# Kernel tuning notes

Hardware: AMD Instinct MI355X
Metric: run time of the kernel (lower is better)

## Reference

```python
import jax, jax.numpy as jnp
import numpy as np

N, D, R, NB = 50000, 128, 10, 4  # nodes, hidden, relations(with reverse), bases
E, NC = 800000, 12
LN_EPS = 1e-5


def _ln(x, g, b):
    m = x.mean(-1, keepdims=True)
    v = ((x - m) ** 2).mean(-1, keepdims=True)
    return (x - m) / jnp.sqrt(v + LN_EPS) * g + b


def _rgcn_conv(x, comp, bases, root, bias, src, dst, etype):
    # basis decomposition: W[r] = sum_b comp[r,b] * bases[b]
    W = jnp.einsum('rb,bio->rio', comp, bases)            # [R, D, D]
    xt = jnp.einsum('ni,rio->rno', x, W)                  # [R, N, D]
    msg = xt[etype, src]                                  # [E, D] gather
    seg = etype * N + dst                                 # per-(relation, dst) segments
    sums = jax.ops.segment_sum(msg, seg, num_segments=R * N)
    cnt = jax.ops.segment_sum(jnp.ones((msg.shape[0],), x.dtype), seg, num_segments=R * N)
    mean = sums / jnp.maximum(cnt, 1.0)[:, None]          # per-relation mean aggregation
    agg = mean.reshape(R, N, D).sum(0)                    # sum over relations
    return agg + x @ root + bias


def setup_inputs() -> dict:
    key = jax.random.key(0)
    ks = jax.random.split(key, 24)
    s = 0.02
    inp = {
        'edge_index': jax.random.randint(ks[0], (2, E), 0, N),
        'edge_type': jax.random.randint(ks[1], (E,), 0, R),
        'node_indices': jax.random.randint(ks[2], (8192,), 0, N),
        'file_feats': jax.random.normal(ks[3], (20000, 256), jnp.float32),
        'file_idx': jnp.arange(20000, dtype=jnp.int64),
        'domain_feats': jax.random.normal(ks[4], (15000, 128), jnp.float32),
        'domain_idx': jnp.arange(20000, 35000, dtype=jnp.int64),
        'ip_feats': jax.random.normal(ks[5], (10000, 64), jnp.float32),
        'ip_idx': jnp.arange(35000, 45000, dtype=jnp.int64),
        'fallback_emb': jax.random.normal(ks[6], (N, D), jnp.float32) * s,
        'Wf': jax.random.normal(ks[7], (256, D), jnp.float32) * s, 'bf': jnp.zeros((D,), jnp.float32),
        'Wd': jax.random.normal(ks[8], (128, D), jnp.float32) * s, 'bd': jnp.zeros((D,), jnp.float32),
        'Wi': jax.random.normal(ks[9], (64, D), jnp.float32) * s, 'bi': jnp.zeros((D,), jnp.float32),
        'comp1': jax.random.normal(ks[10], (R, NB), jnp.float32) * s,
        'bases1': jax.random.normal(ks[11], (NB, D, D), jnp.float32) * s,
        'root1': jax.random.normal(ks[12], (D, D), jnp.float32) * s, 'bias1': jnp.zeros((D,), jnp.float32),
        'comp2': jax.random.normal(ks[13], (R, NB), jnp.float32) * s,
        'bases2': jax.random.normal(ks[14], (NB, D, D), jnp.float32) * s,
        'root2': jax.random.normal(ks[15], (D, D), jnp.float32) * s, 'bias2': jnp.zeros((D,), jnp.float32),
        'ln1_g': jnp.ones((D,), jnp.float32), 'ln1_b': jnp.zeros((D,), jnp.float32),
        'ln2_g': jnp.ones((D,), jnp.float32), 'ln2_b': jnp.zeros((D,), jnp.float32),
        'Wc1': jax.random.normal(ks[16], (D, D), jnp.float32) * s, 'bc1': jnp.zeros((D,), jnp.float32),
        'Wc2': jax.random.normal(ks[17], (D, NC), jnp.float32) * s, 'bc2': jnp.zeros((NC,), jnp.float32),
    }
    return inp


def reference(edge_index, edge_type, node_indices, file_feats, file_idx, domain_feats,
              domain_idx, ip_feats, ip_idx, fallback_emb, Wf, bf, Wd, bd, Wi, bi,
              comp1, bases1, root1, bias1, comp2, bases2, root2, bias2,
              ln1_g, ln1_b, ln2_g, ln2_b, Wc1, bc1, Wc2, bc2):
    src, dst = edge_index[0], edge_index[1]
    # build node features: fallback embedding overwritten by typed projections
    x = fallback_emb
    x = x.at[file_idx].set(file_feats @ Wf + bf)
    x = x.at[domain_idx].set(domain_feats @ Wd + bd)
    x = x.at[ip_idx].set(ip_feats @ Wi + bi)
    h = _rgcn_conv(x, comp1, bases1, root1, bias1, src, dst, edge_type)
    h = jax.nn.relu(_ln(h, ln1_g, ln1_b))  # dropout is identity at eval
    h = _rgcn_conv(h, comp2, bases2, root2, bias2, src, dst, edge_type)
    h = _ln(h, ln2_g, ln2_b)
    h = h[node_indices]
    h = jax.nn.relu(h @ Wc1 + bc1)
    return h @ Wc2 + bc2
```

## Files before the change

kernel.cpp:

```cpp
#include <hip/hip_runtime.h>

#define D 128
#define R_REL 10
#define NBASE 4
#define NC 12
#define LN_EPS 1e-5f

typedef __attribute__((ext_vector_type(8))) short short8;
typedef __attribute__((ext_vector_type(4))) float f32x4;

static __device__ __forceinline__ unsigned short f2bf(float f) {
    unsigned u = __float_as_uint(f);
    unsigned r = (u + 0x7FFFu + ((u >> 16) & 1u)) >> 16;
    return (unsigned short)r;
}

__global__ void k_copy_bf(const float4* __restrict__ src, uint2* __restrict__ dst, int n4) {
    int i = blockIdx.x * blockDim.x + threadIdx.x;
    if (i < n4) {
        float4 v = src[i];
        uint2 o;
        o.x = (unsigned)f2bf(v.x) | ((unsigned)f2bf(v.y) << 16);
        o.y = (unsigned)f2bf(v.z) | ((unsigned)f2bf(v.w) << 16);
        dst[i] = o;
    }
}

__global__ void k_proj8(const float* __restrict__ feats, const float* __restrict__ W,
                        const float* __restrict__ bias, const int* __restrict__ idx,
                        unsigned short* __restrict__ xb, int M, int K) {
    __shared__ float lds[8 * 256];
    int m0 = blockIdx.x * 8;
    int rows = M - m0; if (rows > 8) rows = 8;
    for (int i = threadIdx.x; i < rows * K; i += 128) {
        int r = i / K, k = i - r * K;
        lds[r * K + k] = feats[(size_t)(m0 + r) * K + k];
    }
    __syncthreads();
    int o = threadIdx.x;
    float bz = bias[o];
    float acc[8];
#pragma unroll
    for (int r = 0; r < 8; ++r) acc[r] = bz;
    for (int k = 0; k < K; ++k) {
        float wv = W[k * D + o];
#pragma unroll
        for (int r = 0; r < 8; ++r) acc[r] = fmaf(lds[r * K + k], wv, acc[r]);
    }
#pragma unroll
    for (int r = 0; r < 8; ++r) {
        if (r < rows) xb[(size_t)idx[m0 + r] * D + o] = f2bf(acc[r]);
    }
}

__global__ void k_deg(const int* __restrict__ ei, int* __restrict__ deg, int E) {
    int e = blockIdx.x * blockDim.x + threadIdx.x;
    if (e < E) atomicAdd(&deg[ei[E + e]], 1);
}

#define SCAN_B 256
__global__ void k_scan1(const int* __restrict__ deg, int* __restrict__ off,
                        int* __restrict__ bsum, int n) {
    __shared__ int lds[SCAN_B];
    int i = blockIdx.x * SCAN_B + threadIdx.x;
    int v = (i < n) ? deg[i] : 0;
    lds[threadIdx.x] = v; __syncthreads();
    for (int s = 1; s < SCAN_B; s <<= 1) {
        int t = (threadIdx.x >= s) ? lds[threadIdx.x - s] : 0;
        __syncthreads();
        lds[threadIdx.x] += t;
        __syncthreads();
    }
    if (i < n) off[i] = lds[threadIdx.x] - v;
    if (threadIdx.x == SCAN_B - 1) bsum[blockIdx.x] = lds[threadIdx.x];
}
__global__ void k_scan2(int* __restrict__ bsum, int nb) {
    __shared__ int lds[SCAN_B];
    int v = (threadIdx.x < nb) ? bsum[threadIdx.x] : 0;
    lds[threadIdx.x] = v; __syncthreads();
    for (int s = 1; s < SCAN_B; s <<= 1) {
        int t = (threadIdx.x >= s) ? lds[threadIdx.x - s] : 0;
        __syncthreads();
        lds[threadIdx.x] += t;
        __syncthreads();
    }
    if (threadIdx.x < nb) bsum[threadIdx.x] = lds[threadIdx.x] - v;
}
__global__ void k_scan3(int* __restrict__ off, const int* __restrict__ bsum,
                        int* __restrict__ cursor, int n) {
    int i = blockIdx.x * SCAN_B + threadIdx.x;
    if (i < n) {
        int o = off[i] + bsum[blockIdx.x];
        off[i] = o;
        cursor[i] = o;
    }
}

__global__ void k_fill(const int* __restrict__ ei, const int* __restrict__ et,
                       int* __restrict__ cursor, unsigned* __restrict__ csr, int E) {
    int e = blockIdx.x * blockDim.x + threadIdx.x;
    if (e < E) {
        int d = ei[E + e];
        int p = atomicAdd(&cursor[d], 1);
        csr[p] = (unsigned)ei[e] | ((unsigned)et[e] << 16);
    }
}

__global__ void k_agg(const unsigned short* __restrict__ xb, const int* __restrict__ off,
                      const int* __restrict__ deg, const unsigned* __restrict__ csr,
                      const float* __restrict__ comp, unsigned short* __restrict__ Zb, int Nn) {
    __shared__ float acc[4][R_REL][D];
    __shared__ float scomp[R_REL * NBASE];
    int w = threadIdx.x >> 6;
    int lane = threadIdx.x & 63;
    if (threadIdx.x < R_REL * NBASE) scomp[threadIdx.x] = comp[threadIdx.x];
    for (int i = threadIdx.x; i < 4 * R_REL * D; i += 256) ((float*)acc)[i] = 0.f;
    __syncthreads();

    int n = blockIdx.x * 4 + w;
    if (n >= Nn) return;

    int start = off[n];
    int dg = deg[n];
    int myCnt = 0;
    float* accw = &acc[w][0][0];
    for (int j = 0; j < dg; ++j) {
        unsigned u = csr[start + j];
        int src = (int)(u & 0xFFFFu);
        int et = (int)(u >> 16);
        unsigned xv = *(const unsigned*)&xb[(size_t)src * D + lane * 2];
        float vx = __uint_as_float(xv << 16);
        float vy = __uint_as_float(xv & 0xFFFF0000u);
        float2 a = *(float2*)&accw[et * D + lane * 2];
        a.x += vx; a.y += vy;
        *(float2*)&accw[et * D + lane * 2] = a;
        if (lane == et) myCnt++;
    }
    float inv[R_REL];
#pragma unroll
    for (int r = 0; r < R_REL; ++r) {
        int c = __shfl(myCnt, r, 64);
        inv[r] = (c > 0) ? (1.f / (float)c) : 1.f;
    }
    float2 mean[R_REL];
#pragma unroll
    for (int r = 0; r < R_REL; ++r) {
        float2 a = *(float2*)&accw[r * D + lane * 2];
        mean[r].x = a.x * inv[r];
        mean[r].y = a.y * inv[r];
    }
#pragma unroll
    for (int b = 0; b < NBASE; ++b) {
        float zx = 0.f, zy = 0.f;
#pragma unroll
        for (int r = 0; r < R_REL; ++r) {
            float c = scomp[r * NBASE + b];
            zx = fmaf(c, mean[r].x, zx);
            zy = fmaf(c, mean[r].y, zy);
        }
        unsigned o = (unsigned)f2bf(zx) | ((unsigned)f2bf(zy) << 16);
        *(unsigned*)&Zb[(size_t)n * 512 + b * D + lane * 2] = o;
    }
}

__global__ void k_bt(const float* __restrict__ bases, const float* __restrict__ root,
                     unsigned short* __restrict__ BT) {
    int i = blockIdx.x * 256 + threadIdx.x;
    if (i >= 128 * 640) return;
    int n = i / 640, k = i - n * 640;
    float v = (k < 512) ? bases[(size_t)k * D + n] : root[(size_t)(k - 512) * D + n];
    BT[i] = f2bf(v);
}

__global__ void k_gemm_mfma(const unsigned short* __restrict__ Zb,
                            const unsigned short* __restrict__ xb,
                            const unsigned short* __restrict__ BT,
                            const float* __restrict__ bias,
                            float* __restrict__ P, int M) {
    __shared__ unsigned short As[32 * 40];
    __shared__ unsigned short Bs[128 * 40];
    int t = threadIdx.x;
    int l = t & 63;
    int w = t >> 6;
    int wm = w & 1;
    int wn = (w >> 1) * 64;
    int m0 = blockIdx.x * 32;
    int lrow = l & 15;
    int kq = l >> 4;

    f32x4 acc[4];
#pragma unroll
    for (int ct = 0; ct < 4; ++ct) acc[ct] = (f32x4){0.f, 0.f, 0.f, 0.f};

    int arow = t >> 3, ako = (t & 7) * 4;
    int brow = t >> 1, bko = (t & 1) * 16;
    int arg = m0 + arow; if (arg >= M) arg = M - 1;

    const unsigned short* aFrag = &As[(wm * 16 + lrow) * 40 + kq * 8];

    for (int k0 = 0; k0 < 640; k0 += 32) {
        __syncthreads();
        {
            const unsigned short* src = (k0 < 512)
                ? &Zb[(size_t)arg * 512 + k0 + ako]
                : &xb[(size_t)arg * D + (k0 - 512) + ako];
            *(uint2*)&As[arow * 40 + ako] = *(const uint2*)src;
        }
        {
            const unsigned short* src = &BT[(size_t)brow * 640 + k0 + bko];
            *(uint4*)&Bs[brow * 40 + bko]     = *(const uint4*)src;
            *(uint4*)&Bs[brow * 40 + bko + 8] = *(const uint4*)(src + 8);
        }
        __syncthreads();
        short8 a = *(const short8*)aFrag;
#pragma unroll
        for (int ct = 0; ct < 4; ++ct) {
            short8 b = *(const short8*)&Bs[(wn + ct * 16 + lrow) * 40 + kq * 8];
            acc[ct] = __builtin_amdgcn_mfma_f32_16x16x32_bf16(a, b, acc[ct], 0, 0, 0);
        }
    }

    int r0 = m0 + wm * 16 + kq * 4;
#pragma unroll
    for (int ct = 0; ct < 4; ++ct) {
        int col = wn + ct * 16 + lrow;
        float bv = bias[col];
#pragma unroll
        for (int r = 0; r < 4; ++r) {
            int rg = r0 + r;
            if (rg < M) P[(size_t)rg * D + col] = acc[ct][r] + bv;
        }
    }
}

__global__ void k_lnrelu(const float* __restrict__ P, const float* __restrict__ g,
                         const float* __restrict__ b, unsigned short* __restrict__ hb, int Nn) {
    int w = threadIdx.x >> 6, lane = threadIdx.x & 63;
    int n = blockIdx.x * 4 + w;
    if (n >= Nn) return;
    float2 v = *(const float2*)&P[(size_t)n * D + lane * 2];
    float s = v.x + v.y;
#pragma unroll
    for (int o = 1; o < 64; o <<= 1) s += __shfl_xor(s, o, 64);
    float m = s * (1.f / 128.f);
    float dx = v.x - m, dy = v.y - m;
    float vs = dx * dx + dy * dy;
#pragma unroll
    for (int o = 1; o < 64; o <<= 1) vs += __shfl_xor(vs, o, 64);
    float inv = rsqrtf(vs * (1.f / 128.f) + LN_EPS);
    float2 gg = *(const float2*)&g[lane * 2];
    float2 bb = *(const float2*)&b[lane * 2];
    float ox = fmaxf(dx * inv * gg.x + bb.x, 0.f);
    float oy = fmaxf(dy * inv * gg.y + bb.y, 0.f);
    unsigned o2 = (unsigned)f2bf(ox) | ((unsigned)f2bf(oy) << 16);
    *(unsigned*)&hb[(size_t)n * D + lane * 2] = o2;
}

__global__ void k_final(const float* __restrict__ P2, const int* __restrict__ nidx,
                        const float* __restrict__ g, const float* __restrict__ b,
                        const float* __restrict__ Wc1, const float* __restrict__ bc1,
                        const float* __restrict__ Wc2, const float* __restrict__ bc2,
                        float* __restrict__ out, int M) {
    __shared__ float ln[D];
    __shared__ float t[D];
    __shared__ float red[2];
    int i = blockIdx.x;
    if (i >= M) return;
    int d = threadIdx.x;
    int n = nidx[i];
    float v = P2[(size_t)n * D + d];
    float s = v;
#pragma unroll
    for (int o = 1; o < 64; o <<= 1) s += __shfl_xor(s, o, 64);
    if ((d & 63) == 0) red[d >> 6] = s;
    __syncthreads();
    float m = (red[0] + red[1]) * (1.f / 128.f);
    __syncthreads();
    float dv = v - m;
    float vs = dv * dv;
#pragma unroll
    for (int o = 1; o < 64; o <<= 1) vs += __shfl_xor(vs, o, 64);
    if ((d & 63) == 0) red[d >> 6] = vs;
    __syncthreads();
    float inv = rsqrtf((red[0] + red[1]) * (1.f / 128.f) + LN_EPS);
    ln[d] = dv * inv * g[d] + b[d];
    __syncthreads();
    float a = bc1[d];
    for (int k = 0; k < D; ++k) a = fmaf(ln[k], Wc1[k * D + d], a);
    t[d] = fmaxf(a, 0.f);
    __syncthreads();
    if (d < NC) {
        float o2 = bc2[d];
        for (int k = 0; k < D; ++k) o2 = fmaf(t[k], Wc2[k * NC + d], o2);
        out[(size_t)i * NC + d] = o2;
    }
}

extern "C" void kernel_launch(void* const* d_in, const int* in_sizes, int n_in,
                              void* d_out, int out_size, void* d_ws, size_t ws_size,
                              hipStream_t stream) {
    const int*   edge_index   = (const int*)d_in[0];
    const int*   edge_type    = (const int*)d_in[1];
    const int*   node_indices = (const int*)d_in[2];
    const float* file_feats   = (const float*)d_in[3];
    const int*   file_idx     = (const int*)d_in[4];
    const float* domain_feats = (const float*)d_in[5];
    const int*   domain_idx   = (const int*)d_in[6];
    const float* ip_feats     = (const float*)d_in[7];
    const int*   ip_idx       = (const int*)d_in[8];
    const float* fallback     = (const float*)d_in[9];
    const float* Wf = (const float*)d_in[10]; const float* bf = (const float*)d_in[11];
    const float* Wd = (const float*)d_in[12]; const float* bd = (const float*)d_in[13];
    const float* Wi = (const float*)d_in[14]; const float* bi = (const float*)d_in[15];
    const float* comp1 = (const float*)d_in[16]; const float* bases1 = (const float*)d_in[17];
    const float* root1 = (const float*)d_in[18]; const float* bias1 = (const float*)d_in[19];
    const float* comp2 = (const float*)d_in[20]; const float* bases2 = (const float*)d_in[21];
    const float* root2 = (const float*)d_in[22]; const float* bias2 = (const float*)d_in[23];
    const float* ln1g = (const float*)d_in[24]; const float* ln1b = (const float*)d_in[25];
    const float* ln2g = (const float*)d_in[26]; const float* ln2b = (const float*)d_in[27];
    const float* Wc1 = (const float*)d_in[28]; const float* bc1 = (const float*)d_in[29];
    const float* Wc2 = (const float*)d_in[30]; const float* bc2 = (const float*)d_in[31];

    const int E  = in_sizes[1];
    const int Nn = in_sizes[9] / D;
    const int Mf = in_sizes[4], Kf = in_sizes[3] / Mf;
    const int Md = in_sizes[6], Kd = in_sizes[5] / Md;
    const int Mi = in_sizes[8], Ki = in_sizes[7] / Mi;
    const int Msel = in_sizes[2];

    char* w = (char*)d_ws;
    auto alloc = [&](size_t bytes) {
        char* p = w;
        w += (bytes + 255) & ~(size_t)255;
        return p;
    };
    unsigned short* xb  = (unsigned short*)alloc((size_t)Nn * D * 2);
    unsigned short* h1b = (unsigned short*)alloc((size_t)Nn * D * 2);
    float*          P   = (float*)alloc((size_t)Nn * D * 4);
    unsigned short* Zb  = (unsigned short*)alloc((size_t)Nn * 512 * 2);
    unsigned short* BT1 = (unsigned short*)alloc((size_t)128 * 640 * 2);
    unsigned short* BT2 = (unsigned short*)alloc((size_t)128 * 640 * 2);
    int* deg    = (int*)alloc((size_t)Nn * 4);
    int* off    = (int*)alloc((size_t)Nn * 4);
    int* cursor = (int*)alloc((size_t)Nn * 4);
    int* bsum   = (int*)alloc(1024);
    unsigned* csr = (unsigned*)alloc((size_t)E * 4);

    hipMemsetAsync(deg, 0, (size_t)Nn * 4, stream);

    int n4 = Nn * D / 4;
    k_copy_bf<<<(n4 + 255) / 256, 256, 0, stream>>>((const float4*)fallback, (uint2*)xb, n4);
    k_proj8<<<(Mf + 7) / 8, 128, 0, stream>>>(file_feats, Wf, bf, file_idx, xb, Mf, Kf);
    k_proj8<<<(Md + 7) / 8, 128, 0, stream>>>(domain_feats, Wd, bd, domain_idx, xb, Md, Kd);
    k_proj8<<<(Mi + 7) / 8, 128, 0, stream>>>(ip_feats, Wi, bi, ip_idx, xb, Mi, Ki);

    int nbt = (128 * 640 + 255) / 256;
    k_bt<<<nbt, 256, 0, stream>>>(bases1, root1, BT1);
    k_bt<<<nbt, 256, 0, stream>>>(bases2, root2, BT2);

    k_deg<<<(E + 255) / 256, 256, 0, stream>>>(edge_index, deg, E);
    int nb = (Nn + SCAN_B - 1) / SCAN_B;
    k_scan1<<<nb, SCAN_B, 0, stream>>>(deg, off, bsum, Nn);
    k_scan2<<<1, SCAN_B, 0, stream>>>(bsum, nb);
    k_scan3<<<nb, SCAN_B, 0, stream>>>(off, bsum, cursor, Nn);
    k_fill<<<(E + 255) / 256, 256, 0, stream>>>(edge_index, edge_type, cursor, csr, E);

    int gemmGrid = (Nn + 31) / 32;

    k_agg<<<(Nn + 3) / 4, 256, 0, stream>>>(xb, off, deg, csr, comp1, Zb, Nn);
    k_gemm_mfma<<<gemmGrid, 256, 0, stream>>>(Zb, xb, BT1, bias1, P, Nn);
    k_lnrelu<<<(Nn + 3) / 4, 256, 0, stream>>>(P, ln1g, ln1b, h1b, Nn);

    k_agg<<<(Nn + 3) / 4, 256, 0, stream>>>(h1b, off, deg, csr, comp2, Zb, Nn);
    k_gemm_mfma<<<gemmGrid, 256, 0, stream>>>(Zb, h1b, BT2, bias2, P, Nn);

    k_final<<<Msel, 128, 0, stream>>>(P, node_indices, ln2g, ln2b, Wc1, bc1, Wc2, bc2,
                                      (float*)d_out, Msel);
}
```

Before: 543.7 us.

## Register-accumulate aggregation with prefetch and double-buffer larger GEMM tiles

The aggregation kernel now keeps per-relation sums in registers instead of shared memory. Each wave loads 64 CSR entries cooperatively, broadcasts them with shuffles, and prefetches the next source row's features one step ahead. The GEMM kernel doubles its M tile to 64 rows per block with two MFMA subtiles per wave, and double-buffers LDS so that global loads for the next K step overlap compute on the current one. This adds register pressure and one LDS buffer per block, and the select chain over the relation index costs extra VALU work per edge.

```diff
diff --git a/kernel.cpp b/kernel.cpp
--- a/kernel.cpp
+++ b/kernel.cpp
@@ -109,54 +109,56 @@
 __global__ void k_agg(const unsigned short* __restrict__ xb, const int* __restrict__ off,
                       const int* __restrict__ deg, const unsigned* __restrict__ csr,
                       const float* __restrict__ comp, unsigned short* __restrict__ Zb, int Nn) {
-    __shared__ float acc[4][R_REL][D];
-    __shared__ float scomp[R_REL * NBASE];
     int w = threadIdx.x >> 6;
     int lane = threadIdx.x & 63;
-    if (threadIdx.x < R_REL * NBASE) scomp[threadIdx.x] = comp[threadIdx.x];
-    for (int i = threadIdx.x; i < 4 * R_REL * D; i += 256) ((float*)acc)[i] = 0.f;
-    __syncthreads();
-
     int n = blockIdx.x * 4 + w;
     if (n >= Nn) return;
 
     int start = off[n];
     int dg = deg[n];
+    float ax[R_REL], ay[R_REL];
+#pragma unroll
+    for (int r = 0; r < R_REL; ++r) { ax[r] = 0.f; ay[r] = 0.f; }
     int myCnt = 0;
-    float* accw = &acc[w][0][0];
-    for (int j = 0; j < dg; ++j) {
-        unsigned u = csr[start + j];
-        int src = (int)(u & 0xFFFFu);
-        int et = (int)(u >> 16);
-        unsigned xv = *(const unsigned*)&xb[(size_t)src * D + lane * 2];
-        float vx = __uint_as_float(xv << 16);
-        float vy = __uint_as_float(xv & 0xFFFF0000u);
-        float2 a = *(float2*)&accw[et * D + lane * 2];
-        a.x += vx; a.y += vy;
-        *(float2*)&accw[et * D + lane * 2] = a;
-        if (lane == et) myCnt++;
-    }
+
+    const unsigned* cp = csr + start;
+    for (int j0 = 0; j0 < dg; j0 += 64) {
+        int m = dg - j0; if (m > 64) m = 64;
+        unsigned myU = (j0 + lane < dg) ? cp[j0 + lane] : 0u;
+        unsigned u = __shfl(myU, 0, 64);
+        int src0 = __builtin_amdgcn_readfirstlane((int)(u & 0xFFFFu));
+        unsigned xv = *(const unsigned*)&xb[(size_t)src0 * D + lane * 2];
+        for (int jj = 0; jj < m; ++jj) {
+            unsigned uc = u, xc = xv;
+            if (jj + 1 < m) {
+                u = __shfl(myU, jj + 1, 64);
+                int s2 = (int)(u & 0xFFFFu);
+                xv = *(const unsigned*)&xb[(size_t)s2 * D + lane * 2];
+            }
+            int et = __builtin_amdgcn_readfirstlane((int)(uc >> 16));
+            float vx = __uint_as_float(xc << 16);
+            float vy = __uint_as_float(xc & 0xFFFF0000u);
+#pragma unroll
+            for (int r = 0; r < R_REL; ++r)
+                if (et == r) { ax[r] += vx; ay[r] += vy; }
+            if (lane == et) myCnt++;
+        }
+    }
+
     float inv[R_REL];
 #pragma unroll
     for (int r = 0; r < R_REL; ++r) {
         int c = __shfl(myCnt, r, 64);
         inv[r] = (c > 0) ? (1.f / (float)c) : 1.f;
     }
-    float2 mean[R_REL];
-#pragma unroll
-    for (int r = 0; r < R_REL; ++r) {
-        float2 a = *(float2*)&accw[r * D + lane * 2];
-        mean[r].x = a.x * inv[r];
-        mean[r].y = a.y * inv[r];
-    }
 #pragma unroll
     for (int b = 0; b < NBASE; ++b) {
         float zx = 0.f, zy = 0.f;
 #pragma unroll
         for (int r = 0; r < R_REL; ++r) {
-            float c = scomp[r * NBASE + b];
-            zx = fmaf(c, mean[r].x, zx);
-            zy = fmaf(c, mean[r].y, zy);
+            float cc = comp[r * NBASE + b];
+            zx = fmaf(cc, ax[r] * inv[r], zx);
+            zy = fmaf(cc, ay[r] * inv[r], zy);
         }
         unsigned o = (unsigned)f2bf(zx) | ((unsigned)f2bf(zy) << 16);
         *(unsigned*)&Zb[(size_t)n * 512 + b * D + lane * 2] = o;
@@ -177,58 +179,72 @@
                             const unsigned short* __restrict__ BT,
                             const float* __restrict__ bias,
                             float* __restrict__ P, int M) {
-    __shared__ unsigned short As[32 * 40];
-    __shared__ unsigned short Bs[128 * 40];
+    __shared__ unsigned short As[2][64 * 40];
+    __shared__ unsigned short Bs[2][128 * 40];
     int t = threadIdx.x;
     int l = t & 63;
     int w = t >> 6;
     int wm = w & 1;
     int wn = (w >> 1) * 64;
-    int m0 = blockIdx.x * 32;
+    int m0 = blockIdx.x * 64;
     int lrow = l & 15;
     int kq = l >> 4;
 
-    f32x4 acc[4];
-#pragma unroll
-    for (int ct = 0; ct < 4; ++ct) acc[ct] = (f32x4){0.f, 0.f, 0.f, 0.f};
-
-    int arow = t >> 3, ako = (t & 7) * 4;
+    f32x4 acc[2][4];
+#pragma unroll
+    for (int s = 0; s < 2; ++s)
+#pragma unroll
+        for (int ct = 0; ct < 4; ++ct) acc[s][ct] = (f32x4){0.f, 0.f, 0.f, 0.f};
+
+    int arow = t >> 2, ako = (t & 3) * 8;
     int brow = t >> 1, bko = (t & 1) * 16;
     int arg = m0 + arow; if (arg >= M) arg = M - 1;
 
-    const unsigned short* aFrag = &As[(wm * 16 + lrow) * 40 + kq * 8];
-
+    uint4 aR, bR0, bR1;
+    auto gload = [&](int k0) {
+        const unsigned short* asrc = (k0 < 512)
+            ? &Zb[(size_t)arg * 512 + k0 + ako]
+            : &xb[(size_t)arg * D + (k0 - 512) + ako];
+        aR = *(const uint4*)asrc;
+        const unsigned short* bsrc = &BT[(size_t)brow * 640 + k0 + bko];
+        bR0 = *(const uint4*)bsrc;
+        bR1 = *(const uint4*)(bsrc + 8);
+    };
+    auto sstore = [&](int p) {
+        *(uint4*)&As[p][arow * 40 + ako] = aR;
+        *(uint4*)&Bs[p][brow * 40 + bko] = bR0;
+        *(uint4*)&Bs[p][brow * 40 + bko + 8] = bR1;
+    };
+
+    gload(0);
+    sstore(0);
+    int p = 0;
     for (int k0 = 0; k0 < 640; k0 += 32) {
         __syncthreads();
-        {
-            const unsigned short* src = (k0 < 512)
-                ? &Zb[(size_t)arg * 512 + k0 + ako]
-                : &xb[(size_t)arg * D + (k0 - 512) + ako];
-            *(uint2*)&As[arow * 40 + ako] = *(const uint2*)src;
+        if (k0 + 32 < 640) gload(k0 + 32);
+        short8 a0 = *(const short8*)&As[p][(wm * 32 + lrow) * 40 + kq * 8];
+        short8 a1 = *(const short8*)&As[p][(wm * 32 + 16 + lrow) * 40 + kq * 8];
+#pragma unroll
+        for (int ct = 0; ct < 4; ++ct) {
+            short8 b = *(const short8*)&Bs[p][(wn + ct * 16 + lrow) * 40 + kq * 8];
+            acc[0][ct] = __builtin_amdgcn_mfma_f32_16x16x32_bf16(a0, b, acc[0][ct], 0, 0, 0);
+            acc[1][ct] = __builtin_amdgcn_mfma_f32_16x16x32_bf16(a1, b, acc[1][ct], 0, 0, 0);
         }
-        {
-            const unsigned short* src = &BT[(size_t)brow * 640 + k0 + bko];
-            *(uint4*)&Bs[brow * 40 + bko]     = *(const uint4*)src;
-            *(uint4*)&Bs[brow * 40 + bko + 8] = *(const uint4*)(src + 8);
-        }
-        __syncthreads();
-        short8 a = *(const short8*)aFrag;
+        if (k0 + 32 < 640) { sstore(p ^ 1); p ^= 1; }
+    }
+
+    int r0 = m0 + wm * 32 + kq * 4;
+#pragma unroll
+    for (int sub = 0; sub < 2; ++sub) {
 #pragma unroll
         for (int ct = 0; ct < 4; ++ct) {
-            short8 b = *(const short8*)&Bs[(wn + ct * 16 + lrow) * 40 + kq * 8];
-            acc[ct] = __builtin_amdgcn_mfma_f32_16x16x32_bf16(a, b, acc[ct], 0, 0, 0);
-        }
-    }
-
-    int r0 = m0 + wm * 16 + kq * 4;
-#pragma unroll
-    for (int ct = 0; ct < 4; ++ct) {
-        int col = wn + ct * 16 + lrow;
-        float bv = bias[col];
-#pragma unroll
-        for (int r = 0; r < 4; ++r) {
-            int rg = r0 + r;
-            if (rg < M) P[(size_t)rg * D + col] = acc[ct][r] + bv;
+            int col = wn + ct * 16 + lrow;
+            float bv = bias[col];
+#pragma unroll
+            for (int r = 0; r < 4; ++r) {
+                int rg = r0 + sub * 16 + r;
+                if (rg < M) P[(size_t)rg * D + col] = acc[sub][ct][r] + bv;
+            }
         }
     }
 }
@@ -365,7 +381,7 @@
     k_scan3<<<nb, SCAN_B, 0, stream>>>(off, bsum, cursor, Nn);
     k_fill<<<(E + 255) / 256, 256, 0, stream>>>(edge_index, edge_type, cursor, csr, E);
 
-    int gemmGrid = (Nn + 31) / 32;
+    int gemmGrid = (Nn + 63) / 64;
 
     k_agg<<<(Nn + 3) / 4, 256, 0, stream>>>(xb, off, deg, csr, comp1, Zb, Nn);
     k_gemm_mfma<<<gemmGrid, 256, 0, stream>>>(Zb, xb, BT1, bias1, P, Nn);
```

Result: slower. 575.6 us (+5.9%).
